# Kernel tuning notes

Hardware: AMD Instinct MI355X
Metric: run time of the kernel (lower is better)

## Reference

```python
import jax, jax.numpy as jnp
import numpy as np

N = 30000   # nodes
E = 480000  # edges
C = 64      # in_channels
NC = 101    # num_classes
K1 = 5      # kernel_size per dim
K = K1 * K1 # 25 kernel weight matrices (dim=2)


def _spline_conv(x, src, dst, pseudo, W, root, bias):
    """SplineConv, degree-1 open B-spline, dim=2, kernel_size=5, aggr='mean'.
    x: [N,C_in], pseudo: [E,2] in [0,1], W: [25,C_in,C_out], root: [C_in,C_out].
    """
    n, c = x.shape
    v = pseudo * (K1 - 1)                       # [E,2] in [0, K1-1]
    bot = jnp.clip(jnp.floor(v), 0, K1 - 1)
    frac = v - bot                              # fractional part
    bot_i = bot.astype(jnp.int32)
    bits = jnp.array([[0, 0], [0, 1], [1, 0], [1, 1]], dtype=jnp.int32)  # S=4 combos
    idx_d = jnp.clip(bot_i[:, None, :] + bits[None, :, :], 0, K1 - 1)    # [E,4,2]
    w_d = jnp.where(bits[None, :, :] == 1, frac[:, None, :], 1.0 - frac[:, None, :])
    B = w_d[..., 0] * w_d[..., 1]               # [E,4] basis weights
    kidx = idx_d[..., 0] * K1 + idx_d[..., 1]   # [E,4] flat kernel index in [0,25)
    msg = B[:, :, None] * x[src][:, None, :]    # [E,4,C] weighted source feats
    seg = (dst[:, None] * K + kidx).reshape(-1) # combined (node,kernel) segment id
    acc = jax.ops.segment_sum(msg.reshape(-1, c), seg, num_segments=n * K)
    acc = acc.reshape(n, K, c)                  # [N,25,C]
    out = jnp.einsum('nkc,kcd->nd', acc, W)     # apply kernel weight matrices
    deg = jax.ops.segment_sum(jnp.ones(dst.shape[0], x.dtype), dst, num_segments=n)
    out = out / jnp.maximum(deg, 1.0)[:, None]  # mean aggregation
    out = out + x @ root                        # root weight
    if bias is not None:
        out = out + bias
    return out


def _bn(x, g, b):
    m = x.mean(0)
    v = x.var(0)
    return g * (x - m) * jax.lax.rsqrt(v + 1e-5) + b


def setup_inputs() -> dict:
    key = jax.random.key(0)
    ks = jax.random.split(key, 30)
    p = lambda k, shape: jax.random.normal(k, shape, jnp.float32) * 0.05
    d = {
        'x': jax.random.normal(ks[0], (N, C), jnp.float32),
        'edge_attr': jax.random.uniform(ks[1], (E, 3), dtype=jnp.float32),
        'src': jax.random.randint(ks[2], (E,), 0, N),
        'dst': jax.random.randint(ks[3], (E,), 0, N),
    }
    for i, name in enumerate(['conv1', 'conv2', 'conv3']):
        d[name + '_W'] = p(ks[4 + 2 * i], (K, C, C))
        d[name + '_root'] = p(ks[5 + 2 * i], (C, C))
        d['norm%d_gamma' % (i + 1)] = jnp.ones((C,), jnp.float32)
        d['norm%d_beta' % (i + 1)] = jnp.zeros((C,), jnp.float32)
    for j, (name, oc) in enumerate([('regr', 4), ('cls', NC), ('obj', 1)]):
        d[name + '_W'] = p(ks[10 + 3 * j], (K, C, oc))
        d[name + '_root'] = p(ks[11 + 3 * j], (C, oc))
        d[name + '_bias'] = jnp.zeros((oc,), jnp.float32)
    return d


def reference(x, edge_attr, src, dst,
              conv1_W, conv1_root, norm1_gamma, norm1_beta,
              conv2_W, conv2_root, norm2_gamma, norm2_beta,
              conv3_W, conv3_root, norm3_gamma, norm3_beta,
              regr_W, regr_root, regr_bias,
              cls_W, cls_root, cls_bias,
              obj_W, obj_root, obj_bias):
    pseudo = edge_attr[:, :2]
    x1 = jax.nn.relu(_bn(_spline_conv(x, src, dst, pseudo, conv1_W, conv1_root, None), norm1_gamma, norm1_beta))
    x2 = jax.nn.relu(_bn(_spline_conv(x1, src, dst, pseudo, conv2_W, conv2_root, None), norm2_gamma, norm2_beta))
    x3 = jax.nn.relu(_bn(_spline_conv(x1, src, dst, pseudo, conv3_W, conv3_root, None), norm3_gamma, norm3_beta))
    reg = _spline_conv(x2, src, dst, pseudo, regr_W, regr_root, regr_bias)
    cls = _spline_conv(x3, src, dst, pseudo, cls_W, cls_root, cls_bias)
    obj = _spline_conv(x3, src, dst, pseudo, obj_W, obj_root, obj_bias)
    return (cls, reg, obj)
```

## Files before the change

kernel.cpp:

```cpp
#include <hip/hip_runtime.h>
#include <hip/hip_bf16.h>

#define NN 30000
#define NE 480000
#define CIN 64
#define KD 1600
#define KT 1664
#define KMAC 13
#define BM 64
#define NBLK 469
#define MROWS (NBLK*BM)
#define NBS 118
#define REG_OFF  (30000*101)
#define OBJ_OFF  (30000*105)

typedef short bf16x8 __attribute__((ext_vector_type(8)));
typedef float f32x4  __attribute__((ext_vector_type(4)));
typedef __attribute__((address_space(3))) unsigned lds_u32;
typedef __attribute__((address_space(1))) const unsigned glb_u32;

__device__ __forceinline__ ushort f2bf(float x) {
    union { float f; unsigned u; } v; v.f = x;
    unsigned r = v.u + 0x7FFFu + ((v.u >> 16) & 1u);
    return (ushort)(r >> 16);
}
__device__ __forceinline__ float bf2f(ushort u) {
    union { unsigned i; float f; } v; v.i = ((unsigned)u) << 16; return v.f;
}

__global__ void k_count(const int* __restrict__ dst, int* __restrict__ deg) {
    int e = blockIdx.x * 256 + threadIdx.x;
    if (e < NE) atomicAdd(&deg[dst[e]], 1);
}

__global__ void k_scan1(const int* __restrict__ deg, int* __restrict__ bsum) {
    __shared__ int sred[4];
    int i = blockIdx.x * 256 + threadIdx.x;
    int v = (i < NN) ? deg[i] : 0;
    #pragma unroll
    for (int o = 32; o >= 1; o >>= 1) v += __shfl_down(v, o);
    int w = threadIdx.x >> 6, l = threadIdx.x & 63;
    if (l == 0) sred[w] = v;
    __syncthreads();
    if (threadIdx.x == 0) bsum[blockIdx.x] = sred[0] + sred[1] + sred[2] + sred[3];
}

__global__ void k_scan2(const int* __restrict__ bsum, int* __restrict__ boff) {
    __shared__ int s[128];
    int t = threadIdx.x;
    int v = (t < NBS) ? bsum[t] : 0;
    s[t] = v; __syncthreads();
    for (int o = 1; o < 128; o <<= 1) {
        int u = (t >= o) ? s[t - o] : 0;
        __syncthreads(); s[t] += u; __syncthreads();
    }
    if (t < NBS) boff[t] = s[t] - v;
}

__global__ void k_scan3(const int* __restrict__ deg, const int* __restrict__ boff,
                        int* __restrict__ rp, int* __restrict__ cur, float* __restrict__ invd) {
    __shared__ int s[256];
    int t = threadIdx.x;
    int i = blockIdx.x * 256 + t;
    int v = (i < NN) ? deg[i] : 0;
    s[t] = v; __syncthreads();
    for (int o = 1; o < 256; o <<= 1) {
        int u = (t >= o) ? s[t - o] : 0;
        __syncthreads(); s[t] += u; __syncthreads();
    }
    int ex = s[t] - v + boff[blockIdx.x];
    if (i < NN) {
        rp[i] = ex; cur[i] = ex;
        invd[i] = 1.f / (float)(v > 0 ? v : 1);
    }
    if (i == NN - 1) rp[NN] = NE;
}

__global__ void k_scatter(const float* __restrict__ ea, const int* __restrict__ src,
                          const int* __restrict__ dst, int* __restrict__ cur,
                          float4* __restrict__ mB, int2* __restrict__ mI) {
    int e = blockIdx.x * 256 + threadIdx.x;
    if (e >= NE) return;
    float p0 = ea[e*3+0], p1 = ea[e*3+1];
    float v0 = p0*4.f, v1 = p1*4.f;
    float b0 = fminf(fmaxf(floorf(v0),0.f),4.f);
    float b1 = fminf(fmaxf(floorf(v1),0.f),4.f);
    float f0 = v0-b0, f1 = v1-b1;
    int i0 = (int)b0, i1 = (int)b1;
    float B00 = (1.f-f0)*(1.f-f1);
    float B01 = (1.f-f0)*f1;
    float B10 = f0*(1.f-f1);
    float B11 = f0*f1;
    int k00 = i0*5 + i1;
    int dn = dst[e];
    int pos = atomicAdd(&cur[dn], 1);
    mB[pos] = make_float4(B00,B01,B10,B11);
    mI[pos] = make_int2(k00, src[e]);
}

__global__ void k_prepw(const float* W1,const float* R1,const float* W2,const float* R2,
                        const float* W3,const float* R3,const float* Wr,const float* Rr,
                        const float* Wc,const float* Rc,const float* Wo,const float* Ro,
                        ushort* T1, ushort* T23, ushort* Tr, ushort* TcTo) {
    int b = blockIdx.x;
    const float* W; const float* R; ushort* T; int od; int col;
    if      (b < 64)  { W=W1; R=R1; T=T1  + (long)b*KT;       od=64;  col=b;     }
    else if (b < 128) { W=W2; R=R2; T=T23 + (long)(b-64)*KT;  od=64;  col=b-64;  }
    else if (b < 192) { W=W3; R=R3; T=T23 + (long)(b-64)*KT;  od=64;  col=b-128; }
    else if (b < 208) { W=Wr; R=Rr; T=Tr  + (long)(b-192)*KT; od=4;   col=b-192; }
    else if (b < 320) { W=Wc; R=Rc; T=TcTo+ (long)(b-208)*KT; od=101; col=b-208; }
    else              { W=Wo; R=Ro; T=TcTo+ (long)(b-208)*KT; od=1;   col=b-320; }
    for (int kc = threadIdx.x; kc < KT; kc += 256) {
        float v = 0.f;
        if (col < od) v = (kc < KD) ? W[(long)kc*od + col] : R[(long)(kc-KD)*od + col];
        T[kc] = f2bf(v);
    }
}

__global__ void k_cvt(const float* __restrict__ x, ushort* __restrict__ xb) {
    int idx = blockIdx.x * 1024 + threadIdx.x;
    if (idx < NN*CIN) xb[idx] = f2bf(x[idx]);
}

__global__ void k_norm(const float* __restrict__ y, const float* __restrict__ st,
                       const float* __restrict__ g, const float* __restrict__ be,
                       ushort* __restrict__ xb) {
    int idx = blockIdx.x * 1024 + threadIdx.x;
    if (idx >= NN*CIN) return;
    int d = idx & 63;
    const float inv_n = 1.f / (float)NN;
    float m = st[d] * inv_n;
    float var = st[64 + d] * inv_n - m * m;
    float a = g[d] * rsqrtf(var + 1e-5f);
    float c = be[d] - m * a;
    xb[idx] = f2bf(fmaxf(y[idx] * a + c, 0.f));
}

#define AGGC(K, A_, B_, C_, D_) case K: A_ += bb.x*xu; B_ += bb.y*xu; C_ += bb.z*xu; D_ += bb.w*xu; break;

__global__ void k_agg(
                      const int* __restrict__ rp, const float4* __restrict__ mB,
                      const int2* __restrict__ mI, const ushort* __restrict__ f,
                      const float* __restrict__ invd, ushort* __restrict__ A) {
    int wid = (blockIdx.x * 256 + threadIdx.x) >> 6;
    wid = __builtin_amdgcn_readfirstlane(wid);
    int l = threadIdx.x & 63;
    if (wid >= NN) return;
    float a00=0.f,a01=0.f,a02=0.f,a03=0.f,a04=0.f;
    float a05=0.f,a06=0.f,a07=0.f,a08=0.f,a09=0.f;
    float a10=0.f,a11=0.f,a12=0.f,a13=0.f,a14=0.f;
    float a15=0.f,a16=0.f,a17=0.f,a18=0.f,a19=0.f;
    float a20=0.f,a21=0.f,a22=0.f,a23=0.f,a24=0.f;
    int beg = rp[wid], end = rp[wid + 1];
    for (int e0 = beg; e0 < end; e0 += 8) {
        int2 m[8];
        #pragma unroll
        for (int u = 0; u < 8; ++u) {
            int e = e0 + u;
            m[u] = mI[(e < end) ? e : beg];
        }
        ushort xv[8];
        #pragma unroll
        for (int u = 0; u < 8; ++u) xv[u] = f[(long)m[u].y * CIN + l];
        __builtin_amdgcn_sched_barrier(0);
        float4 b[8];
        #pragma unroll
        for (int u = 0; u < 8; ++u) {
            int e = e0 + u;
            b[u] = mB[(e < end) ? e : beg];
            if (e >= end) b[u] = make_float4(0,0,0,0);
        }
        __builtin_amdgcn_sched_barrier(0);
        #pragma unroll
        for (int u = 0; u < 8; ++u) {
            float xu = bf2f(xv[u]);
            int k00 = __builtin_amdgcn_readfirstlane(m[u].x);
            float4 bb = b[u];
            switch (k00) {
                AGGC(0,  a00,a01,a05,a06)
                AGGC(1,  a01,a02,a06,a07)
                AGGC(2,  a02,a03,a07,a08)
                AGGC(3,  a03,a04,a08,a09)
                AGGC(5,  a05,a06,a10,a11)
                AGGC(6,  a06,a07,a11,a12)
                AGGC(7,  a07,a08,a12,a13)
                AGGC(8,  a08,a09,a13,a14)
                AGGC(10, a10,a11,a15,a16)
                AGGC(11, a11,a12,a16,a17)
                AGGC(12, a12,a13,a17,a18)
                AGGC(13, a13,a14,a18,a19)
                AGGC(15, a15,a16,a20,a21)
                AGGC(16, a16,a17,a21,a22)
                AGGC(17, a17,a18,a22,a23)
                AGGC(18, a18,a19,a23,a24)
                default: break;
            }
        }
    }
    float s = invd[wid];
    ushort* rb = A + (long)wid * KT + l;
    #define STO(K, V) rb[K*CIN] = f2bf((V) * s);
    STO(0,a00)  STO(1,a01)  STO(2,a02)  STO(3,a03)  STO(4,a04)
    STO(5,a05)  STO(6,a06)  STO(7,a07)  STO(8,a08)  STO(9,a09)
    STO(10,a10) STO(11,a11) STO(12,a12) STO(13,a13) STO(14,a14)
    STO(15,a15) STO(16,a16) STO(17,a17) STO(18,a18) STO(19,a19)
    STO(20,a20) STO(21,a21) STO(22,a22) STO(23,a23) STO(24,a24)
    #undef STO
    rb[KD] = f[(long)wid * CIN + l];
}

template<int MODE>
__global__ void k_gemm(const ushort* __restrict__ A, const ushort* __restrict__ B,
                       float* __restrict__ o0, float* __restrict__ o1,
                       float* __restrict__ s0, float* __restrict__ s1,
                       const float* __restrict__ b0, const float* __restrict__ b1) {
    __shared__ ushort As[2 * 8192];
    f32x4* part = (f32x4*)As;
    const int tid = threadIdx.x, w = tid >> 6, l = tid & 63;
    const int m0 = blockIdx.x * BM;

    int colrow;
    if constexpr (MODE == 0)      colrow = ((w & 3) << 4) + (l & 15);
    else if constexpr (MODE == 2) colrow = (l & 15);
    else                          colrow = (w << 4) + (l & 15);
    const ushort* Bp = B + (long)colrow * KT + ((l >> 4) << 3);

    const int row0 = (w << 3) + (l >> 4);
    const int row1 = row0 + 4;
    const ushort* g0 = A + (long)(m0 + row0) * KT + (((l & 15) ^ (row0 & 7)) << 3);
    const ushort* g1 = A + (long)(m0 + row1) * KT + (((l & 15) ^ (row1 & 7)) << 3);
    ushort* d0 = (ushort*)As + (w << 10);
    ushort* d1 = d0 + 512;

    auto stage = [&](int ks, int bf) {
        const ushort* sA = g0 + ks * 128;
        const ushort* sB = g1 + ks * 128;
        ushort* dA = d0 + (bf << 13);
        ushort* dB = d1 + (bf << 13);
        __builtin_amdgcn_global_load_lds((glb_u32*)sA, (lds_u32*)dA, 16, 0, 0);
        __builtin_amdgcn_global_load_lds((glb_u32*)sB, (lds_u32*)dB, 16, 0, 0);
    };

    f32x4 acc[4];
    #pragma unroll
    for (int m = 0; m < 4; ++m) acc[m] = (f32x4){0.f,0.f,0.f,0.f};

    stage(0, 0);
    __syncthreads();

    int buf = 0;
    for (int ks = 0; ks < KMAC; ++ks) {
        if (ks < KMAC - 1) stage(ks + 1, buf ^ 1);
        bool act;
        if constexpr (MODE == 0)      act = (w < 4) ? (ks < 7) : (ks >= 7);
        else if constexpr (MODE == 2) act = ((ks & 7) == w);
        else                          act = true;
        if (act) {
            const char* Ab = (const char*)As + buf * 16384;
            #pragma unroll
            for (int s = 0; s < 4; ++s) {
                bf16x8 bb = *(const bf16x8*)(Bp + ks * 128 + s * 32);
                #pragma unroll
                for (int m = 0; m < 4; ++m) {
                    int r = (m << 4) + (l & 15);
                    int j = (s << 2) + (l >> 4);
                    bf16x8 a = *(const bf16x8*)(Ab + r * 256 + ((j ^ (r & 7)) << 4));
                    acc[m] = __builtin_amdgcn_mfma_f32_16x16x32_bf16(a, bb, acc[m], 0, 0, 0);
                }
            }
        }
        __syncthreads();
        buf ^= 1;
    }

    auto emit = [&](f32x4* ac, float* out, int ostride, int col, int odcap, float bv, float* stats) {
        float p1 = 0.f, p2 = 0.f;
        #pragma unroll
        for (int m = 0; m < 4; ++m) {
            #pragma unroll
            for (int r = 0; r < 4; ++r) {
                int row = m0 + (m << 4) + ((l >> 4) << 2) + r;
                if (row < NN) {
                    float v = ac[m][r] + bv;
                    if (col < odcap) out[(long)row * ostride + col] = v;
                    p1 += v; p2 += v * v;
                }
            }
        }
        if (stats) {
            p1 += __shfl_down(p1, 32); p2 += __shfl_down(p2, 32);
            p1 += __shfl_down(p1, 16); p2 += __shfl_down(p2, 16);
            if (l < 16) { atomicAdd(&stats[col], p1); atomicAdd(&stats[64 + col], p2); }
        }
    };

    if constexpr (MODE == 0) {
        if (w >= 4) {
            #pragma unroll
            for (int m = 0; m < 4; ++m) part[((w & 3) << 8) + (l << 2) + m] = acc[m];
        }
        __syncthreads();
        if (w < 4) {
            #pragma unroll
            for (int m = 0; m < 4; ++m) acc[m] += part[((w & 3) << 8) + (l << 2) + m];
            emit(acc, o0, 64, ((w & 3) << 4) + (l & 15), 64, 0.f, s0);
        }
    } else if constexpr (MODE == 1) {
        if (w < 4) emit(acc, o0, 64, (w << 4) + (l & 15), 64, 0.f, s0);
        else       emit(acc, o1, 64, ((w - 4) << 4) + (l & 15), 64, 0.f, s1);
    } else if constexpr (MODE == 2) {
        if (w > 0) {
            #pragma unroll
            for (int m = 0; m < 4; ++m) part[((w - 1) << 8) + (l << 2) + m] = acc[m];
        }
        __syncthreads();
        if (w == 0) {
            for (int i = 0; i < 7; ++i) {
                #pragma unroll
                for (int m = 0; m < 4; ++m) acc[m] += part[(i << 8) + (l << 2) + m];
            }
            int col = l & 15;
            emit(acc, o0, 4, col, 4, (col < 4) ? b0[col] : 0.f, nullptr);
        }
    } else {
        if (w < 7) {
            int col = (w << 4) + (l & 15);
            emit(acc, o0, 101, col, 101, (col < 101) ? b0[col] : 0.f, nullptr);
        } else {
            int col = l & 15;
            emit(acc, o1, 1, col, 1, b1[0], nullptr);
        }
    }
}

extern "C" void kernel_launch(void* const* d_in, const int* in_sizes, int n_in,
                              void* d_out, int out_size, void* d_ws, size_t ws_size,
                              hipStream_t stream) {
    const float* x    = (const float*)d_in[0];
    const float* ea   = (const float*)d_in[1];
    const int*   src  = (const int*)d_in[2];
    const int*   dst  = (const int*)d_in[3];
    const float* W1   = (const float*)d_in[4];
    const float* R1   = (const float*)d_in[5];
    const float* g1   = (const float*)d_in[6];
    const float* be1  = (const float*)d_in[7];
    const float* W2   = (const float*)d_in[8];
    const float* R2   = (const float*)d_in[9];
    const float* g2   = (const float*)d_in[10];
    const float* be2  = (const float*)d_in[11];
    const float* W3   = (const float*)d_in[12];
    const float* R3   = (const float*)d_in[13];
    const float* g3   = (const float*)d_in[14];
    const float* be3  = (const float*)d_in[15];
    const float* Wr   = (const float*)d_in[16];
    const float* Rr   = (const float*)d_in[17];
    const float* br   = (const float*)d_in[18];
    const float* Wc   = (const float*)d_in[19];
    const float* Rc   = (const float*)d_in[20];
    const float* bc   = (const float*)d_in[21];
    const float* Wo   = (const float*)d_in[22];
    const float* Ro   = (const float*)d_in[23];
    const float* bo   = (const float*)d_in[24];
    float* out = (float*)d_out;

    char* p = (char*)d_ws;
    auto alloc = [&](size_t bytes) { char* r = p; p += (bytes + 255) & ~(size_t)255; return r; };
    float4* mB   = (float4*)alloc((size_t)NE * 16);
    int2*   mI   = (int2*)  alloc((size_t)NE * 8);
    int*    deg  = (int*)   alloc((size_t)NN * 4);
    int*    rp   = (int*)   alloc((size_t)(NN + 1) * 4);
    int*    cur  = (int*)   alloc((size_t)NN * 4);
    float*  invd = (float*) alloc((size_t)NN * 4);
    int*    bsum = (int*)   alloc((size_t)NBS * 4);
    int*    boff = (int*)   alloc((size_t)NBS * 4);
    ushort* T1   = (ushort*)alloc((size_t)64  * KT * 2);
    ushort* T23  = (ushort*)alloc((size_t)128 * KT * 2);
    ushort* Tr   = (ushort*)alloc((size_t)16  * KT * 2);
    ushort* TcTo = (ushort*)alloc((size_t)128 * KT * 2);
    float*  y1   = (float*) alloc((size_t)NN * CIN * 4);
    float*  y2   = (float*) alloc((size_t)NN * CIN * 4);
    float*  y3   = (float*) alloc((size_t)NN * CIN * 4);
    ushort* xb   = (ushort*)alloc((size_t)NN * CIN * 2);
    float*  stats= (float*) alloc(3 * 128 * 4);
    ushort* A    = (ushort*)alloc((size_t)MROWS * KT * 2);
    float* st1 = stats, *st2 = stats + 128, *st3 = stats + 256;

    hipMemsetAsync(deg, 0, (size_t)NN * 4, stream);
    hipMemsetAsync(stats, 0, 3 * 128 * 4, stream);

    k_count  <<<1875, 256, 0, stream>>>(dst, deg);
    k_scan1  <<<NBS, 256, 0, stream>>>(deg, bsum);
    k_scan2  <<<1, 128, 0, stream>>>(bsum, boff);
    k_scan3  <<<NBS, 256, 0, stream>>>(deg, boff, rp, cur, invd);
    k_scatter<<<1875, 256, 0, stream>>>(ea, src, dst, cur, mB, mI);
    k_prepw  <<<336, 256, 0, stream>>>(W1,R1,W2,R2,W3,R3,Wr,Rr,Wc,Rc,Wo,Ro,T1,T23,Tr,TcTo);
    k_cvt    <<<1875, 1024, 0, stream>>>(x, xb);

    k_agg    <<<7500, 256, 0, stream>>>(rp, mB, mI, xb, invd, A);
    k_gemm<0><<<NBLK, 512, 0, stream>>>(A, T1, y1, nullptr, st1, nullptr, nullptr, nullptr);
    k_norm   <<<1875, 1024, 0, stream>>>(y1, st1, g1, be1, xb);
    k_agg    <<<7500, 256, 0, stream>>>(rp, mB, mI, xb, invd, A);
    k_gemm<1><<<NBLK, 512, 0, stream>>>(A, T23, y2, y3, st2, st3, nullptr, nullptr);
    k_norm   <<<1875, 1024, 0, stream>>>(y2, st2, g2, be2, xb);
    k_agg    <<<7500, 256, 0, stream>>>(rp, mB, mI, xb, invd, A);
    k_gemm<2><<<NBLK, 512, 0, stream>>>(A, Tr, out + REG_OFF, nullptr, nullptr, nullptr, br, nullptr);
    k_norm   <<<1875, 1024, 0, stream>>>(y3, st3, g3, be3, xb);
    k_agg    <<<7500, 256, 0, stream>>>(rp, mB, mI, xb, invd, A);
    k_gemm<3><<<NBLK, 512, 0, stream>>>(A, TcTo, out, out + OBJ_OFF, nullptr, nullptr, bc, bo);
}
```

Baseline: 410.0 us.

## Pack edge metadata into one 16-byte record and triple-buffer GEMM staging

Edge records now carry the kernel index, source id and bf16 basis weights pre-multiplied by the inverse degree, all in one uint4. This replaces separate float4 and int2 arrays, so the aggregation kernel does one 16-byte load per edge instead of two loads, and the per-node scaling moves out of k_agg. The GEMM switches from double to triple buffering with explicit vmcnt waits and raw barriers, so each K-slab is prefetched two steps ahead, and B fragments are loaded before staging is issued. The cost is lower basis-weight precision (bf16) and extra LDS use.

```diff
diff --git a/kernel.cpp b/kernel.cpp
--- a/kernel.cpp
+++ b/kernel.cpp
@@ -27,6 +27,15 @@
 __device__ __forceinline__ float bf2f(ushort u) {
     union { unsigned i; float f; } v; v.i = ((unsigned)u) << 16; return v.f;
 }
+__device__ __forceinline__ float bflo(unsigned u) {
+    union { unsigned i; float f; } v; v.i = u << 16; return v.f;
+}
+__device__ __forceinline__ float bfhi(unsigned u) {
+    union { unsigned i; float f; } v; v.i = u & 0xFFFF0000u; return v.f;
+}
+
+#define WAITV2 asm volatile("s_waitcnt vmcnt(2)" ::: "memory")
+#define WAITV0 asm volatile("s_waitcnt vmcnt(0)" ::: "memory")
 
 __global__ void k_count(const int* __restrict__ dst, int* __restrict__ deg) {
     int e = blockIdx.x * 256 + threadIdx.x;
@@ -78,7 +87,7 @@
 
 __global__ void k_scatter(const float* __restrict__ ea, const int* __restrict__ src,
                           const int* __restrict__ dst, int* __restrict__ cur,
-                          float4* __restrict__ mB, int2* __restrict__ mI) {
+                          const float* __restrict__ invd, uint4* __restrict__ mE) {
     int e = blockIdx.x * 256 + threadIdx.x;
     if (e >= NE) return;
     float p0 = ea[e*3+0], p1 = ea[e*3+1];
@@ -87,15 +96,17 @@
     float b1 = fminf(fmaxf(floorf(v1),0.f),4.f);
     float f0 = v0-b0, f1 = v1-b1;
     int i0 = (int)b0, i1 = (int)b1;
-    float B00 = (1.f-f0)*(1.f-f1);
-    float B01 = (1.f-f0)*f1;
-    float B10 = f0*(1.f-f1);
-    float B11 = f0*f1;
+    int dn = dst[e];
+    float s = invd[dn];
+    float B00 = (1.f-f0)*(1.f-f1)*s;
+    float B01 = (1.f-f0)*f1*s;
+    float B10 = f0*(1.f-f1)*s;
+    float B11 = f0*f1*s;
     int k00 = i0*5 + i1;
-    int dn = dst[e];
     int pos = atomicAdd(&cur[dn], 1);
-    mB[pos] = make_float4(B00,B01,B10,B11);
-    mI[pos] = make_int2(k00, src[e]);
+    unsigned w01 = (unsigned)f2bf(B00) | ((unsigned)f2bf(B01) << 16);
+    unsigned w23 = (unsigned)f2bf(B10) | ((unsigned)f2bf(B11) << 16);
+    mE[pos] = make_uint4((unsigned)k00 | ((unsigned)src[e] << 8), w01, w23, 0u);
 }
 
 __global__ void k_prepw(const float* W1,const float* R1,const float* W2,const float* R2,
@@ -136,12 +147,11 @@
     xb[idx] = f2bf(fmaxf(y[idx] * a + c, 0.f));
 }
 
-#define AGGC(K, A_, B_, C_, D_) case K: A_ += bb.x*xu; B_ += bb.y*xu; C_ += bb.z*xu; D_ += bb.w*xu; break;
+#define AGGC(K, A_, B_, C_, D_) case K: A_ += b0v*xu; B_ += b1v*xu; C_ += b2v*xu; D_ += b3v*xu; break;
 
 __global__ void k_agg(
-                      const int* __restrict__ rp, const float4* __restrict__ mB,
-                      const int2* __restrict__ mI, const ushort* __restrict__ f,
-                      const float* __restrict__ invd, ushort* __restrict__ A) {
+                      const int* __restrict__ rp, const uint4* __restrict__ mE,
+                      const ushort* __restrict__ f, ushort* __restrict__ A) {
     int wid = (blockIdx.x * 256 + threadIdx.x) >> 6;
     wid = __builtin_amdgcn_readfirstlane(wid);
     int l = threadIdx.x & 63;
@@ -153,29 +163,23 @@
     float a20=0.f,a21=0.f,a22=0.f,a23=0.f,a24=0.f;
     int beg = rp[wid], end = rp[wid + 1];
     for (int e0 = beg; e0 < end; e0 += 8) {
-        int2 m[8];
+        uint4 m[8];
         #pragma unroll
         for (int u = 0; u < 8; ++u) {
             int e = e0 + u;
-            m[u] = mI[(e < end) ? e : beg];
+            m[u] = mE[(e < end) ? e : beg];
+            if (e >= end) { m[u].y = 0u; m[u].z = 0u; }
         }
         ushort xv[8];
         #pragma unroll
-        for (int u = 0; u < 8; ++u) xv[u] = f[(long)m[u].y * CIN + l];
-        __builtin_amdgcn_sched_barrier(0);
-        float4 b[8];
-        #pragma unroll
-        for (int u = 0; u < 8; ++u) {
-            int e = e0 + u;
-            b[u] = mB[(e < end) ? e : beg];
-            if (e >= end) b[u] = make_float4(0,0,0,0);
-        }
+        for (int u = 0; u < 8; ++u) xv[u] = f[(long)(m[u].x >> 8) * CIN + l];
         __builtin_amdgcn_sched_barrier(0);
         #pragma unroll
         for (int u = 0; u < 8; ++u) {
             float xu = bf2f(xv[u]);
-            int k00 = __builtin_amdgcn_readfirstlane(m[u].x);
-            float4 bb = b[u];
+            float b0v = bflo(m[u].y), b1v = bfhi(m[u].y);
+            float b2v = bflo(m[u].z), b3v = bfhi(m[u].z);
+            int k00 = __builtin_amdgcn_readfirstlane(m[u].x & 0xFFu);
             switch (k00) {
                 AGGC(0,  a00,a01,a05,a06)
                 AGGC(1,  a01,a02,a06,a07)
@@ -197,9 +201,8 @@
             }
         }
     }
-    float s = invd[wid];
     ushort* rb = A + (long)wid * KT + l;
-    #define STO(K, V) rb[K*CIN] = f2bf((V) * s);
+    #define STO(K, V) rb[K*CIN] = f2bf(V);
     STO(0,a00)  STO(1,a01)  STO(2,a02)  STO(3,a03)  STO(4,a04)
     STO(5,a05)  STO(6,a06)  STO(7,a07)  STO(8,a08)  STO(9,a09)
     STO(10,a10) STO(11,a11) STO(12,a12) STO(13,a13) STO(14,a14)
@@ -214,7 +217,7 @@
                        float* __restrict__ o0, float* __restrict__ o1,
                        float* __restrict__ s0, float* __restrict__ s1,
                        const float* __restrict__ b0, const float* __restrict__ b1) {
-    __shared__ ushort As[2 * 8192];
+    __shared__ ushort As[3 * 8192];
     f32x4* part = (f32x4*)As;
     const int tid = threadIdx.x, w = tid >> 6, l = tid & 63;
     const int m0 = blockIdx.x * BM;
@@ -235,10 +238,8 @@
     auto stage = [&](int ks, int bf) {
         const ushort* sA = g0 + ks * 128;
         const ushort* sB = g1 + ks * 128;
-        ushort* dA = d0 + (bf << 13);
-        ushort* dB = d1 + (bf << 13);
-        __builtin_amdgcn_global_load_lds((glb_u32*)sA, (lds_u32*)dA, 16, 0, 0);
-        __builtin_amdgcn_global_load_lds((glb_u32*)sB, (lds_u32*)dB, 16, 0, 0);
+        __builtin_amdgcn_global_load_lds((glb_u32*)sA, (lds_u32*)(d0 + bf * 8192), 16, 0, 0);
+        __builtin_amdgcn_global_load_lds((glb_u32*)sB, (lds_u32*)(d1 + bf * 8192), 16, 0, 0);
     };
 
     f32x4 acc[4];
@@ -246,31 +247,39 @@
     for (int m = 0; m < 4; ++m) acc[m] = (f32x4){0.f,0.f,0.f,0.f};
 
     stage(0, 0);
-    __syncthreads();
-
-    int buf = 0;
+    stage(1, 1);
+    WAITV2;
+    __builtin_amdgcn_s_barrier();
+    __builtin_amdgcn_sched_barrier(0);
+
     for (int ks = 0; ks < KMAC; ++ks) {
-        if (ks < KMAC - 1) stage(ks + 1, buf ^ 1);
+        const int bufc = ks % 3;
         bool act;
         if constexpr (MODE == 0)      act = (w < 4) ? (ks < 7) : (ks >= 7);
         else if constexpr (MODE == 2) act = ((ks & 7) == w);
         else                          act = true;
         if (act) {
-            const char* Ab = (const char*)As + buf * 16384;
+            bf16x8 bb[4];
+            #pragma unroll
+            for (int s = 0; s < 4; ++s) bb[s] = *(const bf16x8*)(Bp + ks * 128 + s * 32);
+            if (ks + 2 < KMAC) stage(ks + 2, (ks + 2) % 3);
+            const char* Ab = (const char*)As + bufc * 16384;
             #pragma unroll
             for (int s = 0; s < 4; ++s) {
-                bf16x8 bb = *(const bf16x8*)(Bp + ks * 128 + s * 32);
                 #pragma unroll
                 for (int m = 0; m < 4; ++m) {
                     int r = (m << 4) + (l & 15);
                     int j = (s << 2) + (l >> 4);
                     bf16x8 a = *(const bf16x8*)(Ab + r * 256 + ((j ^ (r & 7)) << 4));
-                    acc[m] = __builtin_amdgcn_mfma_f32_16x16x32_bf16(a, bb, acc[m], 0, 0, 0);
+                    acc[m] = __builtin_amdgcn_mfma_f32_16x16x32_bf16(a, bb[s], acc[m], 0, 0, 0);
                 }
             }
-        }
-        __syncthreads();
-        buf ^= 1;
+        } else {
+            if (ks + 2 < KMAC) stage(ks + 2, (ks + 2) % 3);
+        }
+        if (ks < KMAC - 2) { WAITV2; } else { WAITV0; }
+        __builtin_amdgcn_s_barrier();
+        __builtin_amdgcn_sched_barrier(0);
     }
 
     auto emit = [&](f32x4* ac, float* out, int ostride, int col, int odcap, float bv, float* stats) {
@@ -365,8 +374,7 @@
 
     char* p = (char*)d_ws;
     auto alloc = [&](size_t bytes) { char* r = p; p += (bytes + 255) & ~(size_t)255; return r; };
-    float4* mB   = (float4*)alloc((size_t)NE * 16);
-    int2*   mI   = (int2*)  alloc((size_t)NE * 8);
+    uint4*  mE   = (uint4*) alloc((size_t)NE * 16);
     int*    deg  = (int*)   alloc((size_t)NN * 4);
     int*    rp   = (int*)   alloc((size_t)(NN + 1) * 4);
     int*    cur  = (int*)   alloc((size_t)NN * 4);
@@ -392,19 +400,19 @@
     k_scan1  <<<NBS, 256, 0, stream>>>(deg, bsum);
     k_scan2  <<<1, 128, 0, stream>>>(bsum, boff);
     k_scan3  <<<NBS, 256, 0, stream>>>(deg, boff, rp, cur, invd);
-    k_scatter<<<1875, 256, 0, stream>>>(ea, src, dst, cur, mB, mI);
+    k_scatter<<<1875, 256, 0, stream>>>(ea, src, dst, cur, invd, mE);
     k_prepw  <<<336, 256, 0, stream>>>(W1,R1,W2,R2,W3,R3,Wr,Rr,Wc,Rc,Wo,Ro,T1,T23,Tr,TcTo);
     k_cvt    <<<1875, 1024, 0, stream>>>(x, xb);
 
-    k_agg    <<<7500, 256, 0, stream>>>(rp, mB, mI, xb, invd, A);
+    k_agg    <<<7500, 256, 0, stream>>>(rp, mE, xb, A);
     k_gemm<0><<<NBLK, 512, 0, stream>>>(A, T1, y1, nullptr, st1, nullptr, nullptr, nullptr);
     k_norm   <<<1875, 1024, 0, stream>>>(y1, st1, g1, be1, xb);
-    k_agg    <<<7500, 256, 0, stream>>>(rp, mB, mI, xb, invd, A);
+    k_agg    <<<7500, 256, 0, stream>>>(rp, mE, xb, A);
     k_gemm<1><<<NBLK, 512, 0, stream>>>(A, T23, y2, y3, st2, st3, nullptr, nullptr);
     k_norm   <<<1875, 1024, 0, stream>>>(y2, st2, g2, be2, xb);
-    k_agg    <<<7500, 256, 0, stream>>>(rp, mB, mI, xb, invd, A);
+    k_agg    <<<7500, 256, 0, stream>>>(rp, mE, xb, A);
     k_gemm<2><<<NBLK, 512, 0, stream>>>(A, Tr, out + REG_OFF, nullptr, nullptr, nullptr, br, nullptr);
     k_norm   <<<1875, 1024, 0, stream>>>(y3, st3, g3, be3, xb);
-    k_agg    <<<7500, 256, 0, stream>>>(rp, mB, mI, xb, invd, A);
+    k_agg    <<<7500, 256, 0, stream>>>(rp, mE, xb, A);
     k_gemm<3><<<NBLK, 512, 0, stream>>>(A, TcTo, out, out + OBJ_OFF, nullptr, nullptr, bc, bo);
 }
```

Result: no change. 404.7 us (-1.3%).
